# Optimization experiments

Hardware: AMD Instinct MI355X
Metric: run time of the kernel (lower is better)

## Reference

```python
import jax, jax.numpy as jnp
import numpy as np
import math

N_HEADS = 16


def setup_inputs() -> dict:
    key = jax.random.key(0)
    ks = jax.random.split(key, 5)
    B, S, E = 2, 2048, 1024
    scale = 1.0 / math.sqrt(E)
    return {
        "x": jax.random.normal(ks[0], (B, S, E), dtype=jnp.float32),
        "w_in": jax.random.normal(ks[1], (3 * E, E), dtype=jnp.float32) * scale,
        "b_in": jax.random.normal(ks[2], (3 * E,), dtype=jnp.float32) * 0.01,
        "w_out": jax.random.normal(ks[3], (E, E), dtype=jnp.float32) * scale,
        "b_out": jax.random.normal(ks[4], (E,), dtype=jnp.float32) * 0.01,
    }


def reference(x, w_in, b_in, w_out, b_out):
    B, S, E = x.shape
    H = N_HEADS
    d = E // H
    # fused QKV projection: [B,S,3E]
    qkv = x @ w_in.T + b_in
    q, k, v = jnp.split(qkv, 3, axis=-1)
    # [B,S,E] -> [B,H,S,d]
    q = q.reshape(B, S, H, d).transpose(0, 2, 1, 3)
    k = k.reshape(B, S, H, d).transpose(0, 2, 1, 3)
    v = v.reshape(B, S, H, d).transpose(0, 2, 1, 3)
    # scores [B,H,S,S], scaled by 1/sqrt(d_head) (no causal mask: casual_mask=False)
    scores = jnp.einsum("bhqd,bhkd->bhqk", q, k) / jnp.sqrt(jnp.float32(d)).astype(x.dtype)
    w = jax.nn.softmax(scores, axis=-1)
    # attention output [B,H,S,d] -> [B,S,E]
    out = jnp.einsum("bhqk,bhkd->bhqd", w, v)
    out = out.transpose(0, 2, 1, 3).reshape(B, S, E)
    return out @ w_out.T + b_out
```

## Files before the change

### kernel.cpp

```cpp
#include <hip/hip_runtime.h>
#include <cstdint>


typedef __bf16 bf16x8 __attribute__((ext_vector_type(8)));
typedef float f32x4 __attribute__((ext_vector_type(4)));

__device__ __forceinline__ unsigned short f32_to_bf16_rne(float f) {
    unsigned int u = __builtin_bit_cast(unsigned int, f);
    u += 0x7FFF + ((u >> 16) & 1);
    return (unsigned short)(u >> 16);
}

__device__ __forceinline__ unsigned int pack_bf16_trunc(float a, float b) {
    unsigned int ua = __builtin_bit_cast(unsigned int, a);
    unsigned int ub = __builtin_bit_cast(unsigned int, b);
    return __builtin_amdgcn_perm(ub, ua, 0x07060302u);
}

__device__ __forceinline__ void gload16(const void* g, void* l) {
    __builtin_amdgcn_global_load_lds(
        (const __attribute__((address_space(1))) unsigned int*)g,
        (__attribute__((address_space(3))) unsigned int*)l, 16, 0, 0);
}

__global__ void cvt_all(const float* __restrict__ x, const float* __restrict__ wi,
                        const float* __restrict__ wo, unsigned short* __restrict__ xb,
                        unsigned short* __restrict__ wib, unsigned short* __restrict__ wob) {
    int i = blockIdx.x * blockDim.x + threadIdx.x;
    const float* src; unsigned short* dst; int off;
    if (i < 1048576)            { src = x;  dst = xb;  off = i; }
    else if (i < 1048576 + 786432) { src = wi; dst = wib; off = i - 1048576; }
    else                        { src = wo; dst = wob; off = i - (1048576 + 786432); }
    float4 v = ((const float4*)src)[off];
    ushort4 o;
    o.x = f32_to_bf16_rne(v.x); o.y = f32_to_bf16_rne(v.y);
    o.z = f32_to_bf16_rne(v.z); o.w = f32_to_bf16_rne(v.w);
    ((ushort4*)dst)[off] = o;
}

__launch_bounds__(256)
__global__ void gemm_qkv(const unsigned short* __restrict__ X,
                         const unsigned short* __restrict__ W,
                         const float* __restrict__ bias,
                         unsigned short* __restrict__ Qp,
                         unsigned short* __restrict__ Kp,
                         unsigned short* __restrict__ Vt) {
    __shared__ __align__(16) unsigned short As[128 * 32];
    __shared__ __align__(16) unsigned short Bs[128 * 32];
    const int t = threadIdx.x;
    const int w = t >> 6, lane = t & 63, quad = lane >> 4, l16 = lane & 15;
    const int wm = (w >> 1) * 64, wn = (w & 1) * 64;
    const int m0 = blockIdx.y * 128, n0 = blockIdx.x * 128;

    f32x4 acc[4][4] = {};

    for (int kt = 0; kt < 1024; kt += 32) {
        __syncthreads();
#pragma unroll
        for (int i = 0; i < 2; ++i) {
            int c = t + 256 * i;
            int r = c >> 2, cc = (c & 3) * 8;
            gload16(&X[(m0 + r) * 1024 + kt + cc], &As[c * 8]);
            gload16(&W[(n0 + r) * 1024 + kt + cc], &Bs[c * 8]);
        }
        __syncthreads();
        bf16x8 af[4], bw[4];
#pragma unroll
        for (int mi = 0; mi < 4; ++mi)
            af[mi] = *(const bf16x8*)&As[(wm + mi * 16 + l16) * 32 + quad * 8];
#pragma unroll
        for (int ni = 0; ni < 4; ++ni)
            bw[ni] = *(const bf16x8*)&Bs[(wn + ni * 16 + l16) * 32 + quad * 8];
#pragma unroll
        for (int mi = 0; mi < 4; ++mi)
#pragma unroll
            for (int ni = 0; ni < 4; ++ni)
                acc[mi][ni] = __builtin_amdgcn_mfma_f32_16x16x32_bf16(af[mi], bw[ni], acc[mi][ni], 0, 0, 0);
    }

    const float QSCALE = 0.125f * 1.44269504089f;
#pragma unroll
    for (int mi = 0; mi < 4; ++mi) {
#pragma unroll
        for (int ni = 0; ni < 4; ++ni) {
            int col = n0 + wn + ni * 16 + l16;
            float bv = bias[col];
            int which = col >> 10;
            int hc = col & 1023;
            int h = hc >> 6, d = hc & 63;
            int row0 = m0 + wm + mi * 16 + quad * 4;
            int b = row0 >> 11, s0 = row0 & 2047;
            int bh = b * 16 + h;
            if (which == 2) {
                ushort4 pk;
                pk.x = f32_to_bf16_rne(acc[mi][ni][0] + bv);
                pk.y = f32_to_bf16_rne(acc[mi][ni][1] + bv);
                pk.z = f32_to_bf16_rne(acc[mi][ni][2] + bv);
                pk.w = f32_to_bf16_rne(acc[mi][ni][3] + bv);
                *(ushort4*)&Vt[(bh * 64 + d) * 2048 + s0] = pk;
            } else if (which == 0) {
#pragma unroll
                for (int r = 0; r < 4; ++r)
                    Qp[(bh * 2048 + s0 + r) * 64 + d] =
                        f32_to_bf16_rne((acc[mi][ni][r] + bv) * QSCALE);
            } else {
#pragma unroll
                for (int r = 0; r < 4; ++r)
                    Kp[(bh * 2048 + s0 + r) * 64 + d] = f32_to_bf16_rne(acc[mi][ni][r] + bv);
            }
        }
    }
}

#define LDP 72
__launch_bounds__(256, 2)
__global__ void attn(const unsigned short* __restrict__ Qp, const unsigned short* __restrict__ Kp,
                     const unsigned short* __restrict__ Vt, unsigned short* __restrict__ A2) {
    __shared__ __align__(16) unsigned short Ks[2][64 * LDP];
    __shared__ __align__(16) unsigned short Vs[2][64 * LDP];
    __shared__ __align__(16) unsigned short Ps[4][32 * LDP];
    const int t = threadIdx.x, w = t >> 6, lane = t & 63, quad = lane >> 4, l16 = lane & 15;
    const int bh = blockIdx.x;
    const int qb = blockIdx.y;
    const unsigned short* Qh = Qp + bh * (2048 * 64);
    const unsigned short* Kh = Kp + bh * (2048 * 64);
    const unsigned short* Vh = Vt + bh * (64 * 2048);

    bf16x8 qf[2][2];
#pragma unroll
    for (int nq = 0; nq < 2; ++nq)
#pragma unroll
        for (int ks = 0; ks < 2; ++ks) {
            int row = qb * 128 + w * 32 + nq * 16 + l16;
            qf[nq][ks] = *(const bf16x8*)&Qh[row * 64 + ks * 32 + quad * 8];
        }

    const int sr0 = t >> 3, sc0 = (t & 7) * 8;
    const int sr1 = (t + 256) >> 3, sc1 = sc0;

    f32x4 o_acc[4][2] = {};
    float l_lane[2] = {0.f, 0.f};

    {
        *(uint4*)&Ks[0][sr0 * LDP + sc0] = *(const uint4*)&Kh[sr0 * 64 + sc0];
        *(uint4*)&Ks[0][sr1 * LDP + sc1] = *(const uint4*)&Kh[sr1 * 64 + sc1];
        *(uint4*)&Vs[0][sr0 * LDP + sc0] = *(const uint4*)&Vh[sr0 * 2048 + sc0];
        *(uint4*)&Vs[0][sr1 * LDP + sc1] = *(const uint4*)&Vh[sr1 * 2048 + sc1];
    }

    int cur = 0;
    for (int it = 0; it < 32; ++it) {
        __syncthreads();
        uint4 kn0, kn1, vn0, vn1;
        const bool pfetch = (it != 31);
        if (pfetch) {
            int ktn = (it + 1) * 64;
            kn0 = *(const uint4*)&Kh[(ktn + sr0) * 64 + sc0];
            kn1 = *(const uint4*)&Kh[(ktn + sr1) * 64 + sc1];
            vn0 = *(const uint4*)&Vh[sr0 * 2048 + ktn + sc0];
            vn1 = *(const uint4*)&Vh[sr1 * 2048 + ktn + sc1];
        }
        const unsigned short* Kc = Ks[cur];
        const unsigned short* Vc = Vs[cur];

        f32x4 s_acc[4][2] = {};
#pragma unroll
        for (int ks = 0; ks < 2; ++ks)
#pragma unroll
            for (int mi = 0; mi < 4; ++mi) {
                bf16x8 kf = *(const bf16x8*)&Kc[(mi * 16 + l16) * LDP + ks * 32 + quad * 8];
#pragma unroll
                for (int nq = 0; nq < 2; ++nq)
                    s_acc[mi][nq] = __builtin_amdgcn_mfma_f32_16x16x32_bf16(kf, qf[nq][ks], s_acc[mi][nq], 0, 0, 0);
            }

#pragma unroll
        for (int nq = 0; nq < 2; ++nq) {
            float rsum = 0.f;
#pragma unroll
            for (int mi = 0; mi < 4; ++mi) {
                float p0 = exp2f(s_acc[mi][nq][0]);
                float p1 = exp2f(s_acc[mi][nq][1]);
                float p2 = exp2f(s_acc[mi][nq][2]);
                float p3 = exp2f(s_acc[mi][nq][3]);
                rsum += (p0 + p1) + (p2 + p3);
                uint2 pk;
                pk.x = pack_bf16_trunc(p0, p1);
                pk.y = pack_bf16_trunc(p2, p3);
                *(uint2*)&Ps[w][(nq * 16 + l16) * LDP + mi * 16 + quad * 4] = pk;
            }
            l_lane[nq] += rsum;
        }

        __asm__ volatile("s_waitcnt lgkmcnt(0)" ::: "memory");

        bf16x8 pf[2][2];
#pragma unroll
        for (int nq = 0; nq < 2; ++nq)
#pragma unroll
            for (int ks = 0; ks < 2; ++ks)
                pf[nq][ks] = *(const bf16x8*)&Ps[w][(nq * 16 + l16) * LDP + ks * 32 + quad * 8];
#pragma unroll
        for (int ks = 0; ks < 2; ++ks)
#pragma unroll
            for (int mi = 0; mi < 4; ++mi) {
                bf16x8 vf = *(const bf16x8*)&Vc[(mi * 16 + l16) * LDP + ks * 32 + quad * 8];
#pragma unroll
                for (int nq = 0; nq < 2; ++nq)
                    o_acc[mi][nq] = __builtin_amdgcn_mfma_f32_16x16x32_bf16(vf, pf[nq][ks], o_acc[mi][nq], 0, 0, 0);
            }

        if (pfetch) {
            *(uint4*)&Ks[cur ^ 1][sr0 * LDP + sc0] = kn0;
            *(uint4*)&Ks[cur ^ 1][sr1 * LDP + sc1] = kn1;
            *(uint4*)&Vs[cur ^ 1][sr0 * LDP + sc0] = vn0;
            *(uint4*)&Vs[cur ^ 1][sr1 * LDP + sc1] = vn1;
        }
        cur ^= 1;
    }

    const int b = bh >> 4, h = bh & 15;
#pragma unroll
    for (int nq = 0; nq < 2; ++nq) {
        float l = l_lane[nq];
        l += __shfl_xor(l, 16);
        l += __shfl_xor(l, 32);
        float rl = 1.0f / l;
        int s = qb * 128 + w * 32 + nq * 16 + l16;
        int tok = b * 2048 + s;
#pragma unroll
        for (int mi = 0; mi < 4; ++mi) {
            ushort4 o;
            o.x = f32_to_bf16_rne(o_acc[mi][nq][0] * rl);
            o.y = f32_to_bf16_rne(o_acc[mi][nq][1] * rl);
            o.z = f32_to_bf16_rne(o_acc[mi][nq][2] * rl);
            o.w = f32_to_bf16_rne(o_acc[mi][nq][3] * rl);
            *(ushort4*)&A2[tok * 1024 + h * 64 + mi * 16 + quad * 4] = o;
        }
    }
}

__launch_bounds__(256)
__global__ void gemm_out_k(const unsigned short* __restrict__ A, const unsigned short* __restrict__ W,
                           const float* __restrict__ bias, float* __restrict__ out) {
    __shared__ __align__(16) unsigned short As[128 * 32];
    __shared__ __align__(16) unsigned short Bs[64 * 32];
    const int t = threadIdx.x;
    const int w = t >> 6, lane = t & 63, quad = lane >> 4, l16 = lane & 15;
    const int wm = (w >> 1) * 64, wn = (w & 1) * 32;
    const int m0 = blockIdx.y * 128, n0 = blockIdx.x * 64;

    f32x4 acc[4][2] = {};

    for (int kt = 0; kt < 1024; kt += 32) {
        __syncthreads();
#pragma unroll
        for (int i = 0; i < 2; ++i) {
            int c = t + 256 * i;
            int r = c >> 2, cc = (c & 3) * 8;
            gload16(&A[(m0 + r) * 1024 + kt + cc], &As[c * 8]);
        }
        {
            int c = t;
            int r = c >> 2, cc = (c & 3) * 8;
            gload16(&W[(n0 + r) * 1024 + kt + cc], &Bs[c * 8]);
        }
        __syncthreads();
        bf16x8 af[4], bw[2];
#pragma unroll
        for (int mi = 0; mi < 4; ++mi)
            af[mi] = *(const bf16x8*)&As[(wm + mi * 16 + l16) * 32 + quad * 8];
#pragma unroll
        for (int ni = 0; ni < 2; ++ni)
            bw[ni] = *(const bf16x8*)&Bs[(wn + ni * 16 + l16) * 32 + quad * 8];
#pragma unroll
        for (int mi = 0; mi < 4; ++mi)
#pragma unroll
            for (int ni = 0; ni < 2; ++ni)
                acc[mi][ni] = __builtin_amdgcn_mfma_f32_16x16x32_bf16(af[mi], bw[ni], acc[mi][ni], 0, 0, 0);
    }

#pragma unroll
    for (int mi = 0; mi < 4; ++mi)
#pragma unroll
        for (int ni = 0; ni < 2; ++ni) {
            int col = n0 + wn + ni * 16 + l16;
            float bv = bias[col];
#pragma unroll
            for (int r = 0; r < 4; ++r) {
                int row = m0 + wm + mi * 16 + quad * 4 + r;
                out[row * 1024 + col] = acc[mi][ni][r] + bv;
            }
        }
}

extern "C" void kernel_launch(void* const* d_in, const int* in_sizes, int n_in,
                              void* d_out, int out_size, void* d_ws, size_t ws_size,
                              hipStream_t stream) {
    const float* x     = (const float*)d_in[0];
    const float* w_in  = (const float*)d_in[1];
    const float* b_in  = (const float*)d_in[2];
    const float* w_out = (const float*)d_in[3];
    const float* b_out = (const float*)d_in[4];
    float* out = (float*)d_out;

    char* ws = (char*)d_ws;
    unsigned short* xb  = (unsigned short*)(ws);
    unsigned short* wib = (unsigned short*)(ws + 8388608);
    unsigned short* wob = (unsigned short*)(ws + 14680064);
    unsigned short* Qp  = (unsigned short*)(ws + 16777216);
    unsigned short* Kp  = (unsigned short*)(ws + 25165824);
    unsigned short* Vt  = (unsigned short*)(ws + 33554432);
    unsigned short* A2  = (unsigned short*)(ws + 41943040);

    cvt_all<<<8192, 256, 0, stream>>>(x, w_in, w_out, xb, wib, wob);
    gemm_qkv<<<dim3(24, 32), 256, 0, stream>>>(xb, wib, b_in, Qp, Kp, Vt);
    attn<<<dim3(32, 16), 256, 0, stream>>>(Qp, Kp, Vt, A2);
    gemm_out_k<<<dim3(16, 32), 256, 0, stream>>>(A2, wob, b_out, out);
}
```

Before: 221.0 us.

## Keep softmax probabilities in registers for PV MFMA and halve attention block size

The attention kernel no longer writes P tiles to shared memory and reads them back. The exp'd probabilities are packed straight into register operands for 16x16x16 bf16 MFMAs, whose operand layout matches the score accumulator layout. Blocks shrink to 128 threads covering 64 query rows, with a doubled grid, so each block loads the same K/V tiles with more loads per thread. This removes the LDS round trip and a wait, but it uses the older, lower-throughput MFMA shape and doubles the total K/V tile traffic into LDS.

After: 215.5 us. 1.03x faster.

```diff
diff --git a/kernel.cpp b/kernel.cpp
--- a/kernel.cpp
+++ b/kernel.cpp
@@ -3,6 +3,7 @@
 
 
 typedef __bf16 bf16x8 __attribute__((ext_vector_type(8)));
+typedef short s16x4 __attribute__((ext_vector_type(4)));
 typedef float f32x4 __attribute__((ext_vector_type(4)));
 
 __device__ __forceinline__ unsigned short f32_to_bf16_rne(float f) {
@@ -113,12 +114,11 @@
 }
 
 #define LDP 72
-__launch_bounds__(256, 2)
+__launch_bounds__(128, 2)
 __global__ void attn(const unsigned short* __restrict__ Qp, const unsigned short* __restrict__ Kp,
                      const unsigned short* __restrict__ Vt, unsigned short* __restrict__ A2) {
     __shared__ __align__(16) unsigned short Ks[2][64 * LDP];
     __shared__ __align__(16) unsigned short Vs[2][64 * LDP];
-    __shared__ __align__(16) unsigned short Ps[4][32 * LDP];
     const int t = threadIdx.x, w = t >> 6, lane = t & 63, quad = lane >> 4, l16 = lane & 15;
     const int bh = blockIdx.x;
     const int qb = blockIdx.y;
@@ -131,34 +131,35 @@
     for (int nq = 0; nq < 2; ++nq)
 #pragma unroll
         for (int ks = 0; ks < 2; ++ks) {
-            int row = qb * 128 + w * 32 + nq * 16 + l16;
+            int row = qb * 64 + w * 32 + nq * 16 + l16;
             qf[nq][ks] = *(const bf16x8*)&Qh[row * 64 + ks * 32 + quad * 8];
         }
-
-    const int sr0 = t >> 3, sc0 = (t & 7) * 8;
-    const int sr1 = (t + 256) >> 3, sc1 = sc0;
 
     f32x4 o_acc[4][2] = {};
     float l_lane[2] = {0.f, 0.f};
 
-    {
-        *(uint4*)&Ks[0][sr0 * LDP + sc0] = *(const uint4*)&Kh[sr0 * 64 + sc0];
-        *(uint4*)&Ks[0][sr1 * LDP + sc1] = *(const uint4*)&Kh[sr1 * 64 + sc1];
-        *(uint4*)&Vs[0][sr0 * LDP + sc0] = *(const uint4*)&Vh[sr0 * 2048 + sc0];
-        *(uint4*)&Vs[0][sr1 * LDP + sc1] = *(const uint4*)&Vh[sr1 * 2048 + sc1];
+#pragma unroll
+    for (int i = 0; i < 4; ++i) {
+        int c = t + 128 * i;
+        int r = c >> 3, cc = (c & 7) * 8;
+        *(uint4*)&Ks[0][r * LDP + cc] = *(const uint4*)&Kh[r * 64 + cc];
+        *(uint4*)&Vs[0][r * LDP + cc] = *(const uint4*)&Vh[r * 2048 + cc];
     }
 
     int cur = 0;
     for (int it = 0; it < 32; ++it) {
         __syncthreads();
-        uint4 kn0, kn1, vn0, vn1;
+        uint4 kn[4], vn[4];
         const bool pfetch = (it != 31);
         if (pfetch) {
             int ktn = (it + 1) * 64;
-            kn0 = *(const uint4*)&Kh[(ktn + sr0) * 64 + sc0];
-            kn1 = *(const uint4*)&Kh[(ktn + sr1) * 64 + sc1];
-            vn0 = *(const uint4*)&Vh[sr0 * 2048 + ktn + sc0];
-            vn1 = *(const uint4*)&Vh[sr1 * 2048 + ktn + sc1];
+#pragma unroll
+            for (int i = 0; i < 4; ++i) {
+                int c = t + 128 * i;
+                int r = c >> 3, cc = (c & 7) * 8;
+                kn[i] = *(const uint4*)&Kh[(ktn + r) * 64 + cc];
+                vn[i] = *(const uint4*)&Vh[r * 2048 + ktn + cc];
+            }
         }
         const unsigned short* Kc = Ks[cur];
         const unsigned short* Vc = Vs[cur];
@@ -174,6 +175,7 @@
                     s_acc[mi][nq] = __builtin_amdgcn_mfma_f32_16x16x32_bf16(kf, qf[nq][ks], s_acc[mi][nq], 0, 0, 0);
             }
 
+        s16x4 bq[4][2];
 #pragma unroll
         for (int nq = 0; nq < 2; ++nq) {
             float rsum = 0.f;
@@ -187,34 +189,30 @@
                 uint2 pk;
                 pk.x = pack_bf16_trunc(p0, p1);
                 pk.y = pack_bf16_trunc(p2, p3);
-                *(uint2*)&Ps[w][(nq * 16 + l16) * LDP + mi * 16 + quad * 4] = pk;
+                bq[mi][nq] = __builtin_bit_cast(s16x4, pk);
             }
             l_lane[nq] += rsum;
         }
 
-        __asm__ volatile("s_waitcnt lgkmcnt(0)" ::: "memory");
-
-        bf16x8 pf[2][2];
-#pragma unroll
-        for (int nq = 0; nq < 2; ++nq)
-#pragma unroll
-            for (int ks = 0; ks < 2; ++ks)
-                pf[nq][ks] = *(const bf16x8*)&Ps[w][(nq * 16 + l16) * LDP + ks * 32 + quad * 8];
-#pragma unroll
-        for (int ks = 0; ks < 2; ++ks)
-#pragma unroll
-            for (int mi = 0; mi < 4; ++mi) {
-                bf16x8 vf = *(const bf16x8*)&Vc[(mi * 16 + l16) * LDP + ks * 32 + quad * 8];
+#pragma unroll
+        for (int dm = 0; dm < 4; ++dm)
+#pragma unroll
+            for (int kt4 = 0; kt4 < 4; ++kt4) {
+                s16x4 av = __builtin_bit_cast(s16x4,
+                    *(const uint2*)&Vc[(dm * 16 + l16) * LDP + kt4 * 16 + quad * 4]);
 #pragma unroll
                 for (int nq = 0; nq < 2; ++nq)
-                    o_acc[mi][nq] = __builtin_amdgcn_mfma_f32_16x16x32_bf16(vf, pf[nq][ks], o_acc[mi][nq], 0, 0, 0);
+                    o_acc[dm][nq] = __builtin_amdgcn_mfma_f32_16x16x16bf16_1k(av, bq[kt4][nq], o_acc[dm][nq], 0, 0, 0);
             }
 
         if (pfetch) {
-            *(uint4*)&Ks[cur ^ 1][sr0 * LDP + sc0] = kn0;
-            *(uint4*)&Ks[cur ^ 1][sr1 * LDP + sc1] = kn1;
-            *(uint4*)&Vs[cur ^ 1][sr0 * LDP + sc0] = vn0;
-            *(uint4*)&Vs[cur ^ 1][sr1 * LDP + sc1] = vn1;
+#pragma unroll
+            for (int i = 0; i < 4; ++i) {
+                int c = t + 128 * i;
+                int r = c >> 3, cc = (c & 7) * 8;
+                *(uint4*)&Ks[cur ^ 1][r * LDP + cc] = kn[i];
+                *(uint4*)&Vs[cur ^ 1][r * LDP + cc] = vn[i];
+            }
         }
         cur ^= 1;
     }
@@ -226,16 +224,16 @@
         l += __shfl_xor(l, 16);
         l += __shfl_xor(l, 32);
         float rl = 1.0f / l;
-        int s = qb * 128 + w * 32 + nq * 16 + l16;
+        int s = qb * 64 + w * 32 + nq * 16 + l16;
         int tok = b * 2048 + s;
 #pragma unroll
-        for (int mi = 0; mi < 4; ++mi) {
+        for (int dm = 0; dm < 4; ++dm) {
             ushort4 o;
-            o.x = f32_to_bf16_rne(o_acc[mi][nq][0] * rl);
-            o.y = f32_to_bf16_rne(o_acc[mi][nq][1] * rl);
-            o.z = f32_to_bf16_rne(o_acc[mi][nq][2] * rl);
-            o.w = f32_to_bf16_rne(o_acc[mi][nq][3] * rl);
-            *(ushort4*)&A2[tok * 1024 + h * 64 + mi * 16 + quad * 4] = o;
+            o.x = f32_to_bf16_rne(o_acc[dm][nq][0] * rl);
+            o.y = f32_to_bf16_rne(o_acc[dm][nq][1] * rl);
+            o.z = f32_to_bf16_rne(o_acc[dm][nq][2] * rl);
+            o.w = f32_to_bf16_rne(o_acc[dm][nq][3] * rl);
+            *(ushort4*)&A2[tok * 1024 + h * 64 + dm * 16 + quad * 4] = o;
         }
     }
 }
@@ -315,6 +313,6 @@
 
     cvt_all<<<8192, 256, 0, stream>>>(x, w_in, w_out, xb, wib, wob);
     gemm_qkv<<<dim3(24, 32), 256, 0, stream>>>(xb, wib, b_in, Qp, Kp, Vt);
-    attn<<<dim3(32, 16), 256, 0, stream>>>(Qp, Kp, Vt, A2);
+    attn<<<dim3(32, 32), 128, 0, stream>>>(Qp, Kp, Vt, A2);
     gemm_out_k<<<dim3(16, 32), 256, 0, stream>>>(A2, wob, b_out, out);
 }
```

## Keep softmax probabilities in registers for PV MFMA, drop LDS round-trip

Applied to the files above, without the earlier changes.

Attention no longer writes the exponentiated scores to shared memory and reads them back. The S accumulator layout feeds the PV product directly as the B operand of 16x16x16 bf16 MFMAs, with V fragments read as 4-element chunks. This removes the Ps LDS buffer, its stores, loads and wait. The smaller LDS footprint allows the launch bound to rise to 4 blocks per SM, at the cost of twice as many, smaller MFMA instructions and tighter register limits.

Result: no change. 220.6 us (-0.2%).

```diff
diff --git a/kernel.cpp b/kernel.cpp
--- a/kernel.cpp
+++ b/kernel.cpp
@@ -3,6 +3,7 @@
 
 
 typedef __bf16 bf16x8 __attribute__((ext_vector_type(8)));
+typedef short s16x4 __attribute__((ext_vector_type(4)));
 typedef float f32x4 __attribute__((ext_vector_type(4)));
 
 __device__ __forceinline__ unsigned short f32_to_bf16_rne(float f) {
@@ -113,12 +114,11 @@
 }
 
 #define LDP 72
-__launch_bounds__(256, 2)
+__launch_bounds__(256, 4)
 __global__ void attn(const unsigned short* __restrict__ Qp, const unsigned short* __restrict__ Kp,
                      const unsigned short* __restrict__ Vt, unsigned short* __restrict__ A2) {
     __shared__ __align__(16) unsigned short Ks[2][64 * LDP];
     __shared__ __align__(16) unsigned short Vs[2][64 * LDP];
-    __shared__ __align__(16) unsigned short Ps[4][32 * LDP];
     const int t = threadIdx.x, w = t >> 6, lane = t & 63, quad = lane >> 4, l16 = lane & 15;
     const int bh = blockIdx.x;
     const int qb = blockIdx.y;
@@ -136,7 +136,7 @@
         }
 
     const int sr0 = t >> 3, sc0 = (t & 7) * 8;
-    const int sr1 = (t + 256) >> 3, sc1 = sc0;
+    const int sr1 = sr0 + 32, sc1 = sc0;
 
     f32x4 o_acc[4][2] = {};
     float l_lane[2] = {0.f, 0.f};
@@ -174,6 +174,7 @@
                     s_acc[mi][nq] = __builtin_amdgcn_mfma_f32_16x16x32_bf16(kf, qf[nq][ks], s_acc[mi][nq], 0, 0, 0);
             }
 
+        s16x4 bq[4][2];
 #pragma unroll
         for (int nq = 0; nq < 2; ++nq) {
             float rsum = 0.f;
@@ -187,27 +188,20 @@
                 uint2 pk;
                 pk.x = pack_bf16_trunc(p0, p1);
                 pk.y = pack_bf16_trunc(p2, p3);
-                *(uint2*)&Ps[w][(nq * 16 + l16) * LDP + mi * 16 + quad * 4] = pk;
+                bq[mi][nq] = __builtin_bit_cast(s16x4, pk);
             }
             l_lane[nq] += rsum;
         }
 
-        __asm__ volatile("s_waitcnt lgkmcnt(0)" ::: "memory");
-
-        bf16x8 pf[2][2];
-#pragma unroll
-        for (int nq = 0; nq < 2; ++nq)
-#pragma unroll
-            for (int ks = 0; ks < 2; ++ks)
-                pf[nq][ks] = *(const bf16x8*)&Ps[w][(nq * 16 + l16) * LDP + ks * 32 + quad * 8];
-#pragma unroll
-        for (int ks = 0; ks < 2; ++ks)
-#pragma unroll
-            for (int mi = 0; mi < 4; ++mi) {
-                bf16x8 vf = *(const bf16x8*)&Vc[(mi * 16 + l16) * LDP + ks * 32 + quad * 8];
+#pragma unroll
+        for (int dm = 0; dm < 4; ++dm)
+#pragma unroll
+            for (int kt4 = 0; kt4 < 4; ++kt4) {
+                s16x4 av = __builtin_bit_cast(s16x4,
+                    *(const uint2*)&Vc[(dm * 16 + l16) * LDP + kt4 * 16 + quad * 4]);
 #pragma unroll
                 for (int nq = 0; nq < 2; ++nq)
-                    o_acc[mi][nq] = __builtin_amdgcn_mfma_f32_16x16x32_bf16(vf, pf[nq][ks], o_acc[mi][nq], 0, 0, 0);
+                    o_acc[dm][nq] = __builtin_amdgcn_mfma_f32_16x16x16bf16_1k(av, bq[kt4][nq], o_acc[dm][nq], 0, 0, 0);
             }
 
         if (pfetch) {
@@ -229,13 +223,13 @@
         int s = qb * 128 + w * 32 + nq * 16 + l16;
         int tok = b * 2048 + s;
 #pragma unroll
-        for (int mi = 0; mi < 4; ++mi) {
+        for (int dm = 0; dm < 4; ++dm) {
             ushort4 o;
-            o.x = f32_to_bf16_rne(o_acc[mi][nq][0] * rl);
-            o.y = f32_to_bf16_rne(o_acc[mi][nq][1] * rl);
-            o.z = f32_to_bf16_rne(o_acc[mi][nq][2] * rl);
-            o.w = f32_to_bf16_rne(o_acc[mi][nq][3] * rl);
-            *(ushort4*)&A2[tok * 1024 + h * 64 + mi * 16 + quad * 4] = o;
+            o.x = f32_to_bf16_rne(o_acc[dm][nq][0] * rl);
+            o.y = f32_to_bf16_rne(o_acc[dm][nq][1] * rl);
+            o.z = f32_to_bf16_rne(o_acc[dm][nq][2] * rl);
+            o.w = f32_to_bf16_rne(o_acc[dm][nq][3] * rl);
+            *(ushort4*)&A2[tok * 1024 + h * 64 + dm * 16 + quad * 4] = o;
         }
     }
 }
```
